# Optimization experiments

Hardware: AMD Instinct MI355X
Metric: run time of the kernel (lower is better)

The kernel has to match this reference:

```python
import jax, jax.numpy as jnp
import numpy as np

H_HEADS = 32
KV_HEADS = 8
HEAD_DIM = 128
HIDDEN = 2048
EPS = 1e-6


def rms_norm(x, w):
    # normalize over last dim (head_dim)
    var = jnp.mean(jnp.square(x), axis=-1, keepdims=True)
    return x * jax.lax.rsqrt(var + EPS) * w


def rotate_half(x):
    x1, x2 = jnp.split(x, 2, axis=-1)
    return jnp.concatenate([-x2, x1], axis=-1)


def setup_inputs() -> dict:
    key = jax.random.key(0)
    ks = jax.random.split(key, 8)
    B, Q, CTX = 1, 1024, 2048
    T = CTX + Q
    hidden_states = jax.random.normal(ks[0], (B, Q, HIDDEN), jnp.float32)
    target_hidden = jax.random.normal(ks[1], (B, CTX, HIDDEN), jnp.float32)
    # RoPE tables over the full concatenated length
    inv_freq = 1.0 / (10000.0 ** (np.arange(0, HEAD_DIM, 2, dtype=np.float32) / HEAD_DIM))
    pos = np.arange(T, dtype=np.float32)
    freqs = np.outer(pos, inv_freq)                     # [T, hd/2]
    emb = np.concatenate([freqs, freqs], axis=-1)       # [T, hd]
    cos = jnp.asarray(np.cos(emb))[None]                # [1, T, hd]
    sin = jnp.asarray(np.sin(emb))[None]
    # custom mask: context fully visible, causal within noise block
    noise_causal = jnp.tril(jnp.ones((Q, Q), bool))
    mask = jnp.concatenate([jnp.ones((Q, CTX), bool), noise_causal], axis=1)
    attention_mask = mask[None, None]                   # [1,1,Q,T]
    scale = 0.02
    wq = jax.random.normal(ks[2], (H_HEADS * HEAD_DIM, HIDDEN), jnp.float32) * scale
    wk = jax.random.normal(ks[3], (KV_HEADS * HEAD_DIM, HIDDEN), jnp.float32) * scale
    wv = jax.random.normal(ks[4], (KV_HEADS * HEAD_DIM, HIDDEN), jnp.float32) * scale
    wo = jax.random.normal(ks[5], (HIDDEN, H_HEADS * HEAD_DIM), jnp.float32) * scale
    q_norm_w = jnp.ones((HEAD_DIM,), jnp.float32)
    k_norm_w = jnp.ones((HEAD_DIM,), jnp.float32)
    return {"hidden_states": hidden_states, "target_hidden": target_hidden,
            "cos": cos, "sin": sin, "attention_mask": attention_mask,
            "wq": wq, "wk": wk, "wv": wv, "wo": wo,
            "q_norm_w": q_norm_w, "k_norm_w": k_norm_w}


def reference(hidden_states, target_hidden, cos, sin, attention_mask,
              wq, wk, wv, wo, q_norm_w, k_norm_w):
    B, Q, _ = hidden_states.shape
    CTX = target_hidden.shape[1]
    T = CTX + Q
    n_rep = H_HEADS // KV_HEADS
    scaling = HEAD_DIM ** -0.5

    # Q from noise tokens, QK-RMSNorm per head
    q = (hidden_states @ wq.T).reshape(B, Q, H_HEADS, HEAD_DIM)
    q = rms_norm(q, q_norm_w).transpose(0, 2, 1, 3)          # [B,H,Q,hd]

    # K/V: context then noise, concatenated along sequence
    k = jnp.concatenate([target_hidden @ wk.T, hidden_states @ wk.T], axis=1)
    k = rms_norm(k.reshape(B, T, KV_HEADS, HEAD_DIM), k_norm_w).transpose(0, 2, 1, 3)  # [B,Hk,T,hd]
    v = jnp.concatenate([target_hidden @ wv.T, hidden_states @ wv.T], axis=1)
    v = v.reshape(B, T, KV_HEADS, HEAD_DIM).transpose(0, 2, 1, 3)                       # [B,Hk,T,hd]

    # offset RoPE: K uses all T positions, Q uses the last Q positions
    cos_b = cos[:, None]                                      # [B,1,T,hd]
    sin_b = sin[:, None]
    q = q * cos_b[:, :, -Q:, :] + rotate_half(q) * sin_b[:, :, -Q:, :]
    k = k * cos_b + rotate_half(k) * sin_b

    # GQA attention without materializing repeated K/V
    qg = q.reshape(B, KV_HEADS, n_rep, Q, HEAD_DIM)
    scores = jnp.einsum('bgrqd,bgtd->bgrqt', qg, k) * scaling  # [B,Hk,rep,Q,T]
    scores = jnp.where(attention_mask[:, :, None], scores, jnp.finfo(scores.dtype).min)
    probs = jax.nn.softmax(scores, axis=-1)
    out = jnp.einsum('bgrqt,bgtd->bgrqd', probs, v)            # [B,Hk,rep,Q,hd]
    out = out.reshape(B, H_HEADS, Q, HEAD_DIM).transpose(0, 2, 1, 3).reshape(B, Q, H_HEADS * HEAD_DIM)
    return out @ wo.T
```

## Files before the change

### kernel.cpp

```cpp
#include <hip/hip_runtime.h>

#define HIDDEN 2048
#define NQ     1024
#define NCTX   2048
#define NTOT   3072
#define NHEADS 32
#define KVH    8
#define HD     128

typedef __attribute__((ext_vector_type(8))) __bf16 bf16x8;
typedef __attribute__((ext_vector_type(4))) __bf16 bf16x4;
typedef __attribute__((ext_vector_type(4))) float  f32x4;

#define MFMA16(a, b, c) __builtin_amdgcn_mfma_f32_16x16x32_bf16(a, b, c, 0, 0, 0)

#define MSTATIC 12.0f

__device__ __forceinline__ void load_lds16(const void* g, void* l) {
    __builtin_amdgcn_global_load_lds(
        (const __attribute__((address_space(1))) unsigned int*)g,
        (__attribute__((address_space(3))) unsigned int*)l, 16, 0, 0);
}

__global__ __launch_bounds__(256) void conv4_f32_bf16(const float* __restrict__ s0,
                                                      __bf16* __restrict__ d0, int n0,
                                                      const float* __restrict__ s1,
                                                      __bf16* __restrict__ d1, int n1,
                                                      const float* __restrict__ s2,
                                                      __bf16* __restrict__ d2, int n2,
                                                      const float* __restrict__ s3,
                                                      __bf16* __restrict__ d3, int n3) {
    const float* s; __bf16* d; int n;
    switch (blockIdx.y) {
        case 0:  s = s0; d = d0; n = n0; break;
        case 1:  s = s1; d = d1; n = n1; break;
        case 2:  s = s2; d = d2; n = n2; break;
        default: s = s3; d = d3; n = n3; break;
    }
    int i = blockIdx.x * 256 + threadIdx.x;
    int stride = gridDim.x * 256;
    for (; i < n; i += stride) {
        float4 v = ((const float4*)s)[i];
        bf16x4 o;
        o[0] = (__bf16)v.x; o[1] = (__bf16)v.y;
        o[2] = (__bf16)v.z; o[3] = (__bf16)v.w;
        ((bf16x4*)d)[i] = o;
    }
}

__global__ __launch_bounds__(256) void conv_wo(const float* __restrict__ wo,
                                               __bf16* __restrict__ w0,
                                               __bf16* __restrict__ w1) {
    int i = blockIdx.x * 256 + threadIdx.x;
    int stride = gridDim.x * 256;
    for (; i < 2048 * 1024; i += stride) {
        int r = i >> 10, cc = i & 1023;
        float4 v = ((const float4*)wo)[i];
        bf16x4 o;
        o[0] = (__bf16)v.x; o[1] = (__bf16)v.y;
        o[2] = (__bf16)v.z; o[3] = (__bf16)v.w;
        __bf16* dst = (cc & 512) ? w1 : w0;
        *(bf16x4*)(dst + (long)r * 2048 + (cc & 511) * 4) = o;
    }
}

__device__ __forceinline__ void gemm_compute64(const __bf16 (&As)[128][64],
                                               const __bf16 (&Bs)[128][64],
                                               f32x4 (&acc)[4][4],
                                               int wm, int wn, int n16, int quad, int rx) {
#pragma unroll
    for (int ks = 0; ks < 2; ks++) {
        bf16x8 af[4], bfr[4];
#pragma unroll
        for (int i = 0; i < 4; i++)
            af[i] = *(const bf16x8*)&As[wm + i * 16 + n16][((ks * 4 + quad) ^ rx) * 8];
#pragma unroll
        for (int j = 0; j < 4; j++)
            bfr[j] = *(const bf16x8*)&Bs[wn + j * 16 + n16][((ks * 4 + quad) ^ rx) * 8];
#pragma unroll
        for (int i = 0; i < 4; i++)
#pragma unroll
            for (int j = 0; j < 4; j++)
                acc[i][j] = MFMA16(af[i], bfr[j], acc[i][j]);
    }
}

template <typename OutT>
__device__ __forceinline__ void gemm_epilogue(const f32x4 (&acc)[4][4],
                                              OutT* __restrict__ Cblk, int ldc,
                                              int wm, int wn, int n16, int quad) {
#pragma unroll
    for (int i = 0; i < 4; i++)
#pragma unroll
        for (int j = 0; j < 4; j++)
#pragma unroll
            for (int r = 0; r < 4; r++)
                Cblk[(long)(wm + i * 16 + quad * 4 + r) * ldc + wn + j * 16 + n16] =
                    (OutT)acc[i][j][r];
}

template <typename OutT>
__device__ __forceinline__ void gemm128_bb(__bf16 (&As)[128][64], __bf16 (&Bs)[128][64],
                                           const __bf16* __restrict__ Ablk,
                                           const __bf16* __restrict__ Bblk,
                                           OutT* __restrict__ Cblk,
                                           int K, int lda, int ldb, int ldc) {
    const int tid  = threadIdx.x;
    const int lane = tid & 63;
    const int w    = tid >> 6;
    const int n16  = lane & 15;
    const int quad = lane >> 4;
    const int wm = (w & 1) * 64;
    const int wn = (w >> 1) * 64;

    f32x4 acc[4][4];
    const f32x4 fzero = {0.f, 0.f, 0.f, 0.f};
#pragma unroll
    for (int i = 0; i < 4; i++)
#pragma unroll
        for (int j = 0; j < 4; j++) acc[i][j] = fzero;

    const int srow  = w * 32 + (lane >> 3);
    const int sxor  = (lane >> 3) & 7;
    const int scol  = (lane & 7) * 8;
    const int sgcol = ((lane & 7) ^ sxor) * 8;
    const __bf16* Ap = Ablk + (long)srow * lda + sgcol;
    const __bf16* Bp = Bblk + (long)srow * ldb + sgcol;
    const int rx = n16 & 7;

    for (int k0 = 0; k0 < K; k0 += 64) {
#pragma unroll
        for (int i = 0; i < 4; i++) {
            load_lds16(Ap + (long)i * 8 * lda + k0, &As[srow + i * 8][scol]);
            load_lds16(Bp + (long)i * 8 * ldb + k0, &Bs[srow + i * 8][scol]);
        }
        __syncthreads();
        gemm_compute64(As, Bs, acc, wm, wn, n16, quad, rx);
        __syncthreads();
    }
    gemm_epilogue(acc, Cblk, ldc, wm, wn, n16, quad);
}

template <typename OutT>
__device__ __forceinline__ void gemm128_fb(__bf16 (&As)[128][64], __bf16 (&Bs)[128][64],
                                           const __bf16* __restrict__ Ablk,
                                           const float* __restrict__ Bblk,
                                           OutT* __restrict__ Cblk,
                                           int K, int lda, int ldb, int ldc) {
    const int tid  = threadIdx.x;
    const int lane = tid & 63;
    const int w    = tid >> 6;
    const int n16  = lane & 15;
    const int quad = lane >> 4;
    const int wm = (w & 1) * 64;
    const int wn = (w >> 1) * 64;

    f32x4 acc[4][4];
    const f32x4 fzero = {0.f, 0.f, 0.f, 0.f};
#pragma unroll
    for (int i = 0; i < 4; i++)
#pragma unroll
        for (int j = 0; j < 4; j++) acc[i][j] = fzero;

    const int srow  = w * 32 + (lane >> 3);
    const int sxor  = (lane >> 3) & 7;
    const int scol  = (lane & 7) * 8;
    const int sgcol = ((lane & 7) ^ sxor) * 8;
    const __bf16* Ap = Ablk + (long)srow * lda + sgcol;

    const int br0  = tid >> 3;
    const int bxor = br0 & 7;
    const int bgc  = (tid & 7) * 8;
    const int bwc  = ((tid & 7) ^ bxor) * 8;
    const float* Bptr = Bblk + (long)br0 * ldb + bgc;

    const int rx = n16 & 7;
    float4 breg[4][2];

#define LOAD_B(kk)                                                             \
    _Pragma("unroll") for (int i = 0; i < 4; i++) {                            \
        breg[i][0] = *(const float4*)(Bptr + (long)i * 32 * ldb + (kk));       \
        breg[i][1] = *(const float4*)(Bptr + (long)i * 32 * ldb + (kk) + 4);   \
    }

    LOAD_B(0);
    for (int k0 = 0; k0 < K; k0 += 64) {
#pragma unroll
        for (int i = 0; i < 4; i++)
            load_lds16(Ap + (long)i * 8 * lda + k0, &As[srow + i * 8][scol]);
#pragma unroll
        for (int i = 0; i < 4; i++) {
            bf16x8 bb;
            bb[0] = (__bf16)breg[i][0].x; bb[1] = (__bf16)breg[i][0].y;
            bb[2] = (__bf16)breg[i][0].z; bb[3] = (__bf16)breg[i][0].w;
            bb[4] = (__bf16)breg[i][1].x; bb[5] = (__bf16)breg[i][1].y;
            bb[6] = (__bf16)breg[i][1].z; bb[7] = (__bf16)breg[i][1].w;
            *(bf16x8*)&Bs[br0 + i * 32][bwc] = bb;
        }
        if (k0 + 64 < K) LOAD_B(k0 + 64);
        __syncthreads();
        gemm_compute64(As, Bs, acc, wm, wn, n16, quad, rx);
        __syncthreads();
    }
#undef LOAD_B
    gemm_epilogue(acc, Cblk, ldc, wm, wn, n16, quad);
}

__global__ __launch_bounds__(256) void gemm_kvq(const __bf16* __restrict__ tgtb,
                                                const __bf16* __restrict__ hidb,
                                                const __bf16* __restrict__ wkb,
                                                const __bf16* __restrict__ wvb,
                                                const float* __restrict__ wq,
                                                __bf16* __restrict__ kbf,
                                                __bf16* __restrict__ vbf,
                                                __bf16* __restrict__ qbf) {
    __shared__ __bf16 As[128][64];
    __shared__ __bf16 Bs[128][64];
    const int b = blockIdx.x;
    if (b < 384) {
        const int z = b / 192, bb = b - z * 192;
        const int n0 = (bb & 7) * 128, m0 = (bb >> 3) * 128;
        const __bf16* Ap = (m0 < 2048) ? tgtb + (long)m0 * 2048
                                       : hidb + (long)(m0 - 2048) * 2048;
        const __bf16* Bp = (z ? wvb : wkb) + (long)n0 * 2048;
        __bf16* Cp = (z ? vbf : kbf) + (long)m0 * 1024 + n0;
        gemm128_bb<__bf16>(As, Bs, Ap, Bp, Cp, 2048, 2048, 2048, 1024);
    } else {
        const int bb = b - 384;
        const int n0 = (bb & 31) * 128, m0 = (bb >> 5) * 128;
        gemm128_fb<__bf16>(As, Bs, hidb + (long)m0 * 2048, wq + (long)n0 * 2048,
                           qbf + (long)m0 * 4096 + n0, 2048, 2048, 2048, 4096);
    }
}

__global__ __launch_bounds__(256) void gemm_wo2(const __bf16* __restrict__ A,
                                                const __bf16* __restrict__ w0,
                                                const __bf16* __restrict__ w1,
                                                float* __restrict__ out,
                                                float* __restrict__ po1) {
    __shared__ __bf16 As[128][64];
    __shared__ __bf16 Bs[128][64];
    const int m0 = blockIdx.y * 128;
    const int n0 = blockIdx.x * 128;
    const int z  = blockIdx.z;
    const __bf16* Bp = (z ? w1 : w0) + (long)n0 * 2048;
    float* C = (z ? po1 : out) + (long)m0 * 2048 + n0;
    gemm128_bb<float>(As, Bs, A + (long)m0 * 4096 + z * 2048, Bp, C,
                      2048, 4096, 2048, 2048);
}

__global__ __launch_bounds__(256) void add2_inplace(float* __restrict__ out,
                                                    const float* __restrict__ p1, int n4) {
    int i = blockIdx.x * 256 + threadIdx.x;
    int stride = gridDim.x * 256;
    for (; i < n4; i += stride) {
        float4 a = ((const float4*)out)[i];
        float4 b = ((const float4*)p1)[i];
        float4 o;
        o.x = a.x + b.x; o.y = a.y + b.y;
        o.z = a.z + b.z; o.w = a.w + b.w;
        ((float4*)out)[i] = o;
    }
}

__global__ __launch_bounds__(256) void rmsnorm_rope2(__bf16* __restrict__ xq,
                                                     const float* __restrict__ wq,
                                                     __bf16* __restrict__ xk,
                                                     const float* __restrict__ wk,
                                                     const float* __restrict__ cosb,
                                                     const float* __restrict__ sinb) {
    const int z = blockIdx.y;
    __bf16*      x = z ? xk : xq;
    const float* w = z ? wk : wq;
    const int nheads     = z ? 8 : 32;
    const int row_stride = z ? 1024 : 4096;
    const int pos_offset = z ? 0 : 2048;
    const float outscale = z ? 1.0f : 0.08838834764831845f;
    const int nitems     = z ? 3072 * 8 : 1024 * 32;

    int item = blockIdx.x * 4 + (threadIdx.x >> 6);
    int lane = threadIdx.x & 63;
    if (item >= nitems) return;
    int row = item / nheads;
    int head = item - row * nheads;
    __bf16* p = x + (long)row * row_stride + head * HD;

    float x1 = (float)p[lane], x2 = (float)p[lane + 64];
    float ss = x1 * x1 + x2 * x2;
#pragma unroll
    for (int o = 32; o >= 1; o >>= 1) ss += __shfl_xor(ss, o);
    float r = rsqrtf(ss * (1.0f / 128.0f) + 1e-6f) * outscale;

    int pos = pos_offset + row;
    float c1 = cosb[pos * HD + lane], c2 = cosb[pos * HD + lane + 64];
    float s1 = sinb[pos * HD + lane], s2 = sinb[pos * HD + lane + 64];
    float y1 = x1 * r * w[lane];
    float y2 = x2 * r * w[lane + 64];
    p[lane]      = (__bf16)(y1 * c1 - y2 * s1);
    p[lane + 64] = (__bf16)(y2 * c2 + y1 * s2);
}

__global__ __launch_bounds__(256) void transpose_v(const __bf16* __restrict__ v,
                                                   __bf16* __restrict__ vt) {
    __shared__ __bf16 T[64][68];
    const int tid = threadIdx.x;
    const int t0 = blockIdx.x * 64;
    const int d0 = blockIdx.y * 64;
    const int g  = blockIdx.z;
    const __bf16* src = v + (long)t0 * 1024 + g * 128 + d0;
#pragma unroll
    for (int i = 0; i < 4; i++) {
        int idx = tid + i * 256;
        int r = idx >> 4, c4 = (idx & 15) * 4;
        *(bf16x4*)&T[r][c4] = *(const bf16x4*)(src + (long)r * 1024 + c4);
    }
    __syncthreads();
    __bf16* dst = vt + (long)g * 128 * 3072 + (long)d0 * 3072 + t0;
#pragma unroll
    for (int i = 0; i < 4; i++) {
        int idx = tid + i * 256;
        int r = idx >> 4, c4 = (idx & 15) * 4;
        bf16x4 o;
        o[0] = T[c4 + 0][r]; o[1] = T[c4 + 1][r];
        o[2] = T[c4 + 2][r]; o[3] = T[c4 + 3][r];
        *(bf16x4*)(dst + (long)r * 3072 + c4) = o;
    }
}

__global__ __launch_bounds__(256) void flash_attn_splitk(const __bf16* __restrict__ qb,
                                                         const __bf16* __restrict__ kb,
                                                         const __bf16* __restrict__ vtg,
                                                         __bf16* __restrict__ Opart0,
                                                         __bf16* __restrict__ Opart1,
                                                         float* __restrict__ lsum) {
    __shared__ __bf16 KsU[64 * 136];
    __shared__ __bf16 Vs[128][72];
#define KS(r, c) KsU[(r) * 136 + (c)]
#define PS(w_, m_, t_) KsU[(w_) * 2176 + (m_) * 68 + (t_)]

    const int tid  = threadIdx.x;
    const int lane = tid & 63;
    const int w    = tid >> 6;
    const int n    = lane & 15;
    const int quad = lane >> 4;

    const int bid = blockIdx.x;
    const int s   = blockIdx.y;
    const int g  = bid & 7;
    const int jj = bid >> 3;
    const int h  = g * 4 + (jj & 3);
    const int qt = jj >> 2;

    const int qr0 = qt * 128 + w * 16;

    bf16x8 qf[2][4];
#pragma unroll
    for (int mt = 0; mt < 2; mt++) {
        const __bf16* qp = qb + (long)(qr0 + mt * 64 + n) * 4096 + h * 128 + quad * 8;
        qf[mt][0] = *(const bf16x8*)(qp);
        qf[mt][1] = *(const bf16x8*)(qp + 32);
        qf[mt][2] = *(const bf16x8*)(qp + 64);
        qf[mt][3] = *(const bf16x8*)(qp + 96);
    }

    f32x4 O[2][8];
    const f32x4 fzero = {0.f, 0.f, 0.f, 0.f};
#pragma unroll
    for (int mt = 0; mt < 2; mt++)
#pragma unroll
        for (int dt = 0; dt < 8; dt++) O[mt][dt] = fzero;
    float l_loc[2] = {0.f, 0.f};

    const int ntot = 34 + 2 * qt;
    const int half = ntot >> 1;
    const int tbeg = s ? half : 0;
    const int tend = s ? ntot : half;

    const int krr = tid >> 4, kc8 = (tid & 15) * 8;
    const int vrr = tid >> 3, vc8 = (tid & 7) * 8;
    const __bf16* kp = kb + g * 128 + (long)(tbeg * 64 + krr) * 1024 + kc8;
    const __bf16* vp = vtg + (long)g * 128 * 3072 + (long)vrr * 3072 + tbeg * 64 + vc8;

    for (int tt = tbeg; tt < tend; tt++) {
#pragma unroll
        for (int i = 0; i < 4; i++)
            *(bf16x8*)&KS(krr + i * 16, kc8) = *(const bf16x8*)(kp + (long)i * 16 * 1024);
#pragma unroll
        for (int i = 0; i < 4; i++)
            *(bf16x8*)&Vs[vrr + i * 32][vc8] = *(const bf16x8*)(vp + (long)i * 32 * 3072);
        kp += 64 * 1024;
        vp += 64;
        __syncthreads();

        f32x4 S[2][4];
#pragma unroll
        for (int nt = 0; nt < 4; nt++) {
            f32x4 a0 = fzero, a1 = fzero;
#pragma unroll
            for (int ks = 0; ks < 4; ks++) {
                bf16x8 kf = *(const bf16x8*)&KS(nt * 16 + n, ks * 32 + quad * 8);
                a0 = MFMA16(kf, qf[0][ks], a0);
                a1 = MFMA16(kf, qf[1][ks], a1);
            }
            S[0][nt] = a0;
            S[1][nt] = a1;
        }

        if (tt >= ntot - 2) {
            const int t0 = tt * 64;
#pragma unroll
            for (int mt = 0; mt < 2; mt++) {
                const int lim = 2048 + qr0 + mt * 64 + n;
#pragma unroll
                for (int nt = 0; nt < 4; nt++)
#pragma unroll
                    for (int r = 0; r < 4; r++) {
                        int t = t0 + nt * 16 + quad * 4 + r;
                        if (t > lim) S[mt][nt][r] = -1e30f;
                    }
            }
        }

        __syncthreads();

#pragma unroll
        for (int mt = 0; mt < 2; mt++)
#pragma unroll
            for (int nt = 0; nt < 4; nt++)
#pragma unroll
                for (int r = 0; r < 4; r++) {
                    float p = __expf(S[mt][nt][r] - MSTATIC);
                    S[mt][nt][r] = p;
                    l_loc[mt] += p;
                }

#pragma unroll
        for (int mt = 0; mt < 2; mt++)
#pragma unroll
            for (int nt = 0; nt < 4; nt++) {
                bf16x4 pk;
#pragma unroll
                for (int r = 0; r < 4; r++) pk[r] = (__bf16)S[mt][nt][r];
                *(bf16x4*)&PS(w, mt * 16 + n, nt * 16 + quad * 4) = pk;
            }

        bf16x8 pa[2][2];
#pragma unroll
        for (int mt = 0; mt < 2; mt++)
#pragma unroll
            for (int kg = 0; kg < 2; kg++)
                pa[mt][kg] = *(const bf16x8*)&PS(w, mt * 16 + n, kg * 32 + quad * 8);

#pragma unroll
        for (int dt = 0; dt < 8; dt++) {
            bf16x8 vf0 = *(const bf16x8*)&Vs[dt * 16 + n][quad * 8];
            bf16x8 vf1 = *(const bf16x8*)&Vs[dt * 16 + n][32 + quad * 8];
#pragma unroll
            for (int mt = 0; mt < 2; mt++) {
                f32x4 acc = O[mt][dt];
                acc = MFMA16(pa[mt][0], vf0, acc);
                acc = MFMA16(pa[mt][1], vf1, acc);
                O[mt][dt] = acc;
            }
        }
        __syncthreads();
    }

#pragma unroll
    for (int mt = 0; mt < 2; mt++) {
        float sm = l_loc[mt];
        sm += __shfl_xor(sm, 16);
        sm += __shfl_xor(sm, 32);
        l_loc[mt] = sm;
    }

    __bf16* Op = s ? Opart1 : Opart0;
    const long tb = (long)(h * 8 + qt) * 128 * 128;
#pragma unroll
    for (int mt = 0; mt < 2; mt++)
#pragma unroll
        for (int dt = 0; dt < 8; dt++)
#pragma unroll
            for (int r = 0; r < 4; r++)
                Op[tb + (long)(mt * 64 + w * 16 + quad * 4 + r) * 128 + dt * 16 + n] =
                    (__bf16)O[mt][dt][r];
    if (quad == 0) {
        const int lb = (s * 256 + h * 8 + qt) * 128 + w * 16;
#pragma unroll
        for (int mt = 0; mt < 2; mt++)
            lsum[lb + mt * 64 + n] = l_loc[mt];
    }
#undef KS
#undef PS
}

__global__ __launch_bounds__(256) void flash_merge(const __bf16* __restrict__ O0,
                                                   const __bf16* __restrict__ O1,
                                                   const float* __restrict__ lsum,
                                                   __bf16* __restrict__ ob) {
    const int bx = blockIdx.x;
    const int h   = bx >> 4;
    const int r6  = bx & 15;
    const int qt  = r6 >> 1;
    const int sub = r6 & 1;
    const int row  = threadIdx.x >> 2;
    const int cseg = (threadIdx.x & 3) * 32;
    const int mrow = sub * 64 + row;

    const int tilei = h * 8 + qt;
    float inv = 1.0f / (lsum[tilei * 128 + mrow] + lsum[(256 + tilei) * 128 + mrow]);

    const long src = (long)tilei * 128 * 128 + (long)mrow * 128 + cseg;
    __bf16* dst = ob + (long)(qt * 128 + mrow) * 4096 + h * 128 + cseg;
#pragma unroll
    for (int j = 0; j < 4; j++) {
        bf16x8 x0 = *(const bf16x8*)(O0 + src + j * 8);
        bf16x8 x1 = *(const bf16x8*)(O1 + src + j * 8);
        bf16x8 o;
#pragma unroll
        for (int k = 0; k < 8; k++)
            o[k] = (__bf16)(((float)x0[k] + (float)x1[k]) * inv);
        *(bf16x8*)(dst + j * 8) = o;
    }
}

extern "C" void kernel_launch(void* const* d_in, const int* in_sizes, int n_in,
                              void* d_out, int out_size, void* d_ws, size_t ws_size,
                              hipStream_t stream) {
    const float* hidden = (const float*)d_in[0];
    const float* target = (const float*)d_in[1];
    const float* cosb   = (const float*)d_in[2];
    const float* sinb   = (const float*)d_in[3];
    const float* wq = (const float*)d_in[5];
    const float* wk = (const float*)d_in[6];
    const float* wv = (const float*)d_in[7];
    const float* wo = (const float*)d_in[8];
    const float* qw = (const float*)d_in[9];
    const float* kw = (const float*)d_in[10];
    float* out = (float*)d_out;

    char* ws = (char*)d_ws;
    const long MB = 1 << 20;
    __bf16* hidb = (__bf16*)(ws);
    __bf16* tgtb = (__bf16*)(ws + 4 * MB);
    __bf16* wkb  = (__bf16*)(ws + 12 * MB);
    __bf16* wvb  = (__bf16*)(ws + 16 * MB);
    __bf16* kbf  = (__bf16*)(ws + 20 * MB);
    __bf16* vbf  = (__bf16*)(ws + 26 * MB);
    __bf16* vtg  = (__bf16*)(ws + 32 * MB);
    float*  lbuf = (float*)(ws);
    __bf16* Op0  = (__bf16*)(ws + 4 * MB);
    __bf16* Op1  = (__bf16*)(ws + 12 * MB);
    __bf16* attnb= (__bf16*)(ws + 20 * MB);
    __bf16* wob0 = (__bf16*)(ws + 4 * MB);
    __bf16* wob1 = (__bf16*)(ws + 12 * MB);
    float*  po1  = (float*)(ws + 28 * MB);
    __bf16* qbf  = (__bf16*)d_out;

    dim3 blk(256);

    conv4_f32_bf16<<<dim3(1024, 4), blk, 0, stream>>>(
        hidden, hidb, (1024 * 2048) / 4, target, tgtb, (2048 * 2048) / 4,
        wk, wkb, (1024 * 2048) / 4, wv, wvb, (1024 * 2048) / 4);

    gemm_kvq<<<640, blk, 0, stream>>>(tgtb, hidb, wkb, wvb, wq, kbf, vbf, qbf);

    rmsnorm_rope2<<<dim3(8192, 2), blk, 0, stream>>>(qbf, qw, kbf, kw, cosb, sinb);

    transpose_v<<<dim3(48, 2, 8), blk, 0, stream>>>(vbf, vtg);

    flash_attn_splitk<<<dim3(256, 2), blk, 0, stream>>>(qbf, kbf, vtg, Op0, Op1, lbuf);
    flash_merge<<<512, blk, 0, stream>>>(Op0, Op1, lbuf, attnb);

    conv_wo<<<2048, blk, 0, stream>>>(wo, wob0, wob1);
    gemm_wo2<<<dim3(16, 8, 2), blk, 0, stream>>>(attnb, wob0, wob1, out, po1);
    add2_inplace<<<1024, blk, 0, stream>>>(out, po1, (1024 * 2048) / 4);
}
```

Before: 360.0 us.

## Shrink projection GEMM tiles to 128x64 and remap block IDs across XCDs

The K/V/Q projection GEMM and the output-projection GEMM now use 128x64 output tiles instead of 128x128. This doubles the block count (1280 and 512) so the work splits more evenly across the CUs. Linear block IDs are permuted with an XCD-aware stride mapping, and launch bounds request 5 blocks per CU. Each block now reads the A tile twice as often relative to the output it produces, which costs more global and LDS traffic per output element.

```diff
diff --git a/kernel.cpp b/kernel.cpp
--- a/kernel.cpp
+++ b/kernel.cpp
@@ -64,35 +64,35 @@
     }
 }
 
-__device__ __forceinline__ void gemm_compute64(const __bf16 (&As)[128][64],
-                                               const __bf16 (&Bs)[128][64],
-                                               f32x4 (&acc)[4][4],
-                                               int wm, int wn, int n16, int quad, int rx) {
+__device__ __forceinline__ void gemm_compute6432(const __bf16 (&As)[128][64],
+                                                 const __bf16 (&Bs)[64][64],
+                                                 f32x4 (&acc)[4][2],
+                                                 int wm, int wn, int n16, int quad, int rx) {
 #pragma unroll
     for (int ks = 0; ks < 2; ks++) {
-        bf16x8 af[4], bfr[4];
+        bf16x8 af[4], bfr[2];
 #pragma unroll
         for (int i = 0; i < 4; i++)
             af[i] = *(const bf16x8*)&As[wm + i * 16 + n16][((ks * 4 + quad) ^ rx) * 8];
 #pragma unroll
-        for (int j = 0; j < 4; j++)
+        for (int j = 0; j < 2; j++)
             bfr[j] = *(const bf16x8*)&Bs[wn + j * 16 + n16][((ks * 4 + quad) ^ rx) * 8];
 #pragma unroll
         for (int i = 0; i < 4; i++)
 #pragma unroll
-            for (int j = 0; j < 4; j++)
+            for (int j = 0; j < 2; j++)
                 acc[i][j] = MFMA16(af[i], bfr[j], acc[i][j]);
     }
 }
 
 template <typename OutT>
-__device__ __forceinline__ void gemm_epilogue(const f32x4 (&acc)[4][4],
+__device__ __forceinline__ void gemm_epilogue(const f32x4 (&acc)[4][2],
                                               OutT* __restrict__ Cblk, int ldc,
                                               int wm, int wn, int n16, int quad) {
 #pragma unroll
     for (int i = 0; i < 4; i++)
 #pragma unroll
-        for (int j = 0; j < 4; j++)
+        for (int j = 0; j < 2; j++)
 #pragma unroll
             for (int r = 0; r < 4; r++)
                 Cblk[(long)(wm + i * 16 + quad * 4 + r) * ldc + wn + j * 16 + n16] =
@@ -100,67 +100,69 @@
 }
 
 template <typename OutT>
-__device__ __forceinline__ void gemm128_bb(__bf16 (&As)[128][64], __bf16 (&Bs)[128][64],
-                                           const __bf16* __restrict__ Ablk,
-                                           const __bf16* __restrict__ Bblk,
-                                           OutT* __restrict__ Cblk,
-                                           int K, int lda, int ldb, int ldc) {
+__device__ __forceinline__ void gemm6432_bb(__bf16 (&As)[128][64], __bf16 (&Bs)[64][64],
+                                            const __bf16* __restrict__ Ablk,
+                                            const __bf16* __restrict__ Bblk,
+                                            OutT* __restrict__ Cblk,
+                                            int K, int lda, int ldb, int ldc) {
     const int tid  = threadIdx.x;
     const int lane = tid & 63;
     const int w    = tid >> 6;
     const int n16  = lane & 15;
     const int quad = lane >> 4;
     const int wm = (w & 1) * 64;
-    const int wn = (w >> 1) * 64;
-
-    f32x4 acc[4][4];
+    const int wn = (w >> 1) * 32;
+
+    f32x4 acc[4][2];
     const f32x4 fzero = {0.f, 0.f, 0.f, 0.f};
 #pragma unroll
     for (int i = 0; i < 4; i++)
 #pragma unroll
-        for (int j = 0; j < 4; j++) acc[i][j] = fzero;
+        for (int j = 0; j < 2; j++) acc[i][j] = fzero;
 
     const int srow  = w * 32 + (lane >> 3);
+    const int brow  = w * 16 + (lane >> 3);
     const int sxor  = (lane >> 3) & 7;
     const int scol  = (lane & 7) * 8;
     const int sgcol = ((lane & 7) ^ sxor) * 8;
     const __bf16* Ap = Ablk + (long)srow * lda + sgcol;
-    const __bf16* Bp = Bblk + (long)srow * ldb + sgcol;
+    const __bf16* Bp = Bblk + (long)brow * ldb + sgcol;
     const int rx = n16 & 7;
 
     for (int k0 = 0; k0 < K; k0 += 64) {
 #pragma unroll
-        for (int i = 0; i < 4; i++) {
+        for (int i = 0; i < 4; i++)
             load_lds16(Ap + (long)i * 8 * lda + k0, &As[srow + i * 8][scol]);
-            load_lds16(Bp + (long)i * 8 * ldb + k0, &Bs[srow + i * 8][scol]);
-        }
-        __syncthreads();
-        gemm_compute64(As, Bs, acc, wm, wn, n16, quad, rx);
+#pragma unroll
+        for (int i = 0; i < 2; i++)
+            load_lds16(Bp + (long)i * 8 * ldb + k0, &Bs[brow + i * 8][scol]);
+        __syncthreads();
+        gemm_compute6432(As, Bs, acc, wm, wn, n16, quad, rx);
         __syncthreads();
     }
     gemm_epilogue(acc, Cblk, ldc, wm, wn, n16, quad);
 }
 
 template <typename OutT>
-__device__ __forceinline__ void gemm128_fb(__bf16 (&As)[128][64], __bf16 (&Bs)[128][64],
-                                           const __bf16* __restrict__ Ablk,
-                                           const float* __restrict__ Bblk,
-                                           OutT* __restrict__ Cblk,
-                                           int K, int lda, int ldb, int ldc) {
+__device__ __forceinline__ void gemm6432_fb(__bf16 (&As)[128][64], __bf16 (&Bs)[64][64],
+                                            const __bf16* __restrict__ Ablk,
+                                            const float* __restrict__ Bblk,
+                                            OutT* __restrict__ Cblk,
+                                            int K, int lda, int ldb, int ldc) {
     const int tid  = threadIdx.x;
     const int lane = tid & 63;
     const int w    = tid >> 6;
     const int n16  = lane & 15;
     const int quad = lane >> 4;
     const int wm = (w & 1) * 64;
-    const int wn = (w >> 1) * 64;
-
-    f32x4 acc[4][4];
+    const int wn = (w >> 1) * 32;
+
+    f32x4 acc[4][2];
     const f32x4 fzero = {0.f, 0.f, 0.f, 0.f};
 #pragma unroll
     for (int i = 0; i < 4; i++)
 #pragma unroll
-        for (int j = 0; j < 4; j++) acc[i][j] = fzero;
+        for (int j = 0; j < 2; j++) acc[i][j] = fzero;
 
     const int srow  = w * 32 + (lane >> 3);
     const int sxor  = (lane >> 3) & 7;
@@ -175,10 +177,10 @@
     const float* Bptr = Bblk + (long)br0 * ldb + bgc;
 
     const int rx = n16 & 7;
-    float4 breg[4][2];
+    float4 breg[2][2];
 
 #define LOAD_B(kk)                                                             \
-    _Pragma("unroll") for (int i = 0; i < 4; i++) {                            \
+    _Pragma("unroll") for (int i = 0; i < 2; i++) {                            \
         breg[i][0] = *(const float4*)(Bptr + (long)i * 32 * ldb + (kk));       \
         breg[i][1] = *(const float4*)(Bptr + (long)i * 32 * ldb + (kk) + 4);   \
     }
@@ -189,7 +191,7 @@
         for (int i = 0; i < 4; i++)
             load_lds16(Ap + (long)i * 8 * lda + k0, &As[srow + i * 8][scol]);
 #pragma unroll
-        for (int i = 0; i < 4; i++) {
+        for (int i = 0; i < 2; i++) {
             bf16x8 bb;
             bb[0] = (__bf16)breg[i][0].x; bb[1] = (__bf16)breg[i][0].y;
             bb[2] = (__bf16)breg[i][0].z; bb[3] = (__bf16)breg[i][0].w;
@@ -199,54 +201,56 @@
         }
         if (k0 + 64 < K) LOAD_B(k0 + 64);
         __syncthreads();
-        gemm_compute64(As, Bs, acc, wm, wn, n16, quad, rx);
+        gemm_compute6432(As, Bs, acc, wm, wn, n16, quad, rx);
         __syncthreads();
     }
 #undef LOAD_B
     gemm_epilogue(acc, Cblk, ldc, wm, wn, n16, quad);
 }
 
-__global__ __launch_bounds__(256) void gemm_kvq(const __bf16* __restrict__ tgtb,
-                                                const __bf16* __restrict__ hidb,
-                                                const __bf16* __restrict__ wkb,
-                                                const __bf16* __restrict__ wvb,
-                                                const float* __restrict__ wq,
-                                                __bf16* __restrict__ kbf,
-                                                __bf16* __restrict__ vbf,
-                                                __bf16* __restrict__ qbf) {
+__global__ __launch_bounds__(256, 5) void gemm_kvq(const __bf16* __restrict__ tgtb,
+                                                   const __bf16* __restrict__ hidb,
+                                                   const __bf16* __restrict__ wkb,
+                                                   const __bf16* __restrict__ wvb,
+                                                   const float* __restrict__ wq,
+                                                   __bf16* __restrict__ kbf,
+                                                   __bf16* __restrict__ vbf,
+                                                   __bf16* __restrict__ qbf) {
     __shared__ __bf16 As[128][64];
-    __shared__ __bf16 Bs[128][64];
-    const int b = blockIdx.x;
-    if (b < 384) {
-        const int z = b / 192, bb = b - z * 192;
-        const int n0 = (bb & 7) * 128, m0 = (bb >> 3) * 128;
+    __shared__ __bf16 Bs[64][64];
+    const int bid = blockIdx.x;
+    const int b = (bid & 7) * 160 + (bid >> 3);
+    if (b < 768) {
+        const int z = b >> 9 ? 1 : (b >= 384), t = b - z * 384;
+        const int m0 = (t >> 4) * 128, n0 = (t & 15) * 64;
         const __bf16* Ap = (m0 < 2048) ? tgtb + (long)m0 * 2048
                                        : hidb + (long)(m0 - 2048) * 2048;
         const __bf16* Bp = (z ? wvb : wkb) + (long)n0 * 2048;
         __bf16* Cp = (z ? vbf : kbf) + (long)m0 * 1024 + n0;
-        gemm128_bb<__bf16>(As, Bs, Ap, Bp, Cp, 2048, 2048, 2048, 1024);
+        gemm6432_bb<__bf16>(As, Bs, Ap, Bp, Cp, 2048, 2048, 2048, 1024);
     } else {
-        const int bb = b - 384;
-        const int n0 = (bb & 31) * 128, m0 = (bb >> 5) * 128;
-        gemm128_fb<__bf16>(As, Bs, hidb + (long)m0 * 2048, wq + (long)n0 * 2048,
-                           qbf + (long)m0 * 4096 + n0, 2048, 2048, 2048, 4096);
-    }
-}
-
-__global__ __launch_bounds__(256) void gemm_wo2(const __bf16* __restrict__ A,
-                                                const __bf16* __restrict__ w0,
-                                                const __bf16* __restrict__ w1,
-                                                float* __restrict__ out,
-                                                float* __restrict__ po1) {
+        const int t = b - 768;
+        const int m0 = (t >> 6) * 128, n0 = (t & 63) * 64;
+        gemm6432_fb<__bf16>(As, Bs, hidb + (long)m0 * 2048, wq + (long)n0 * 2048,
+                            qbf + (long)m0 * 4096 + n0, 2048, 2048, 2048, 4096);
+    }
+}
+
+__global__ __launch_bounds__(256, 5) void gemm_wo2(const __bf16* __restrict__ A,
+                                                   const __bf16* __restrict__ w0,
+                                                   const __bf16* __restrict__ w1,
+                                                   float* __restrict__ out,
+                                                   float* __restrict__ po1) {
     __shared__ __bf16 As[128][64];
-    __shared__ __bf16 Bs[128][64];
-    const int m0 = blockIdx.y * 128;
-    const int n0 = blockIdx.x * 128;
-    const int z  = blockIdx.z;
+    __shared__ __bf16 Bs[64][64];
+    const int bid = blockIdx.x;
+    const int b = (bid & 7) * 64 + (bid >> 3);
+    const int z = b >> 8, t = b & 255;
+    const int m0 = (t >> 5) * 128, n0 = (t & 31) * 64;
     const __bf16* Bp = (z ? w1 : w0) + (long)n0 * 2048;
     float* C = (z ? po1 : out) + (long)m0 * 2048 + n0;
-    gemm128_bb<float>(As, Bs, A + (long)m0 * 4096 + z * 2048, Bp, C,
-                      2048, 4096, 2048, 2048);
+    gemm6432_bb<float>(As, Bs, A + (long)m0 * 4096 + z * 2048, Bp, C,
+                       2048, 4096, 2048, 2048);
 }
 
 __global__ __launch_bounds__(256) void add2_inplace(float* __restrict__ out,
@@ -563,7 +567,7 @@
         hidden, hidb, (1024 * 2048) / 4, target, tgtb, (2048 * 2048) / 4,
         wk, wkb, (1024 * 2048) / 4, wv, wvb, (1024 * 2048) / 4);
 
-    gemm_kvq<<<640, blk, 0, stream>>>(tgtb, hidb, wkb, wvb, wq, kbf, vbf, qbf);
+    gemm_kvq<<<1280, blk, 0, stream>>>(tgtb, hidb, wkb, wvb, wq, kbf, vbf, qbf);
 
     rmsnorm_rope2<<<dim3(8192, 2), blk, 0, stream>>>(qbf, qw, kbf, kw, cosb, sinb);
 
@@ -573,6 +577,6 @@
     flash_merge<<<512, blk, 0, stream>>>(Op0, Op1, lbuf, attnb);
 
     conv_wo<<<2048, blk, 0, stream>>>(wo, wob0, wob1);
-    gemm_wo2<<<dim3(16, 8, 2), blk, 0, stream>>>(attnb, wob0, wob1, out, po1);
+    gemm_wo2<<<512, blk, 0, stream>>>(attnb, wob0, wob1, out, po1);
     add2_inplace<<<1024, blk, 0, stream>>>(out, po1, (1024 * 2048) / 4);
 }
```

Measured after the change: 358.4 us. No clear change (-0.4%).

## Retile GEMMs to 256x64 blocks, fuse wo conversion, split-K four ways

Applied to the files above, without the earlier changes.

Replaces the 128x128 GEMM tiles with 256x64 tiles, each wave owning 64 rows and sharing a 64-wide B tile, and remaps block indices so neighbouring blocks share A or B panels. The separate wo fp32-to-bf16 conversion kernel is removed. The output projection now reads fp32 wo directly and converts it in registers while staging it into shared memory. The output GEMM is split four ways along K into 512 blocks with four partial buffers summed by a four-way add kernel. This cuts one kernel launch and the round-trip write of converted weights, and raises block count for occupancy, at the cost of extra partial-sum traffic and more A reloads per output tile.

```diff
diff --git a/kernel.cpp b/kernel.cpp
--- a/kernel.cpp
+++ b/kernel.cpp
@@ -48,26 +48,10 @@
     }
 }
 
-__global__ __launch_bounds__(256) void conv_wo(const float* __restrict__ wo,
-                                               __bf16* __restrict__ w0,
-                                               __bf16* __restrict__ w1) {
-    int i = blockIdx.x * 256 + threadIdx.x;
-    int stride = gridDim.x * 256;
-    for (; i < 2048 * 1024; i += stride) {
-        int r = i >> 10, cc = i & 1023;
-        float4 v = ((const float4*)wo)[i];
-        bf16x4 o;
-        o[0] = (__bf16)v.x; o[1] = (__bf16)v.y;
-        o[2] = (__bf16)v.z; o[3] = (__bf16)v.w;
-        __bf16* dst = (cc & 512) ? w1 : w0;
-        *(bf16x4*)(dst + (long)r * 2048 + (cc & 511) * 4) = o;
-    }
-}
-
-__device__ __forceinline__ void gemm_compute64(const __bf16 (&As)[128][64],
-                                               const __bf16 (&Bs)[128][64],
-                                               f32x4 (&acc)[4][4],
-                                               int wm, int wn, int n16, int quad, int rx) {
+__device__ __forceinline__ void gemm_compute256(const __bf16 (&As)[256][64],
+                                                const __bf16 (&Bs)[64][64],
+                                                f32x4 (&acc)[4][4],
+                                                int wm, int n16, int quad, int rx) {
 #pragma unroll
     for (int ks = 0; ks < 2; ks++) {
         bf16x8 af[4], bfr[4];
@@ -76,7 +60,7 @@
             af[i] = *(const bf16x8*)&As[wm + i * 16 + n16][((ks * 4 + quad) ^ rx) * 8];
 #pragma unroll
         for (int j = 0; j < 4; j++)
-            bfr[j] = *(const bf16x8*)&Bs[wn + j * 16 + n16][((ks * 4 + quad) ^ rx) * 8];
+            bfr[j] = *(const bf16x8*)&Bs[j * 16 + n16][((ks * 4 + quad) ^ rx) * 8];
 #pragma unroll
         for (int i = 0; i < 4; i++)
 #pragma unroll
@@ -86,32 +70,31 @@
 }
 
 template <typename OutT>
-__device__ __forceinline__ void gemm_epilogue(const f32x4 (&acc)[4][4],
-                                              OutT* __restrict__ Cblk, int ldc,
-                                              int wm, int wn, int n16, int quad) {
+__device__ __forceinline__ void gemm_epi256(const f32x4 (&acc)[4][4],
+                                            OutT* __restrict__ Cblk, int ldc,
+                                            int wm, int n16, int quad) {
 #pragma unroll
     for (int i = 0; i < 4; i++)
 #pragma unroll
         for (int j = 0; j < 4; j++)
 #pragma unroll
             for (int r = 0; r < 4; r++)
-                Cblk[(long)(wm + i * 16 + quad * 4 + r) * ldc + wn + j * 16 + n16] =
+                Cblk[(long)(wm + i * 16 + quad * 4 + r) * ldc + j * 16 + n16] =
                     (OutT)acc[i][j][r];
 }
 
 template <typename OutT>
-__device__ __forceinline__ void gemm128_bb(__bf16 (&As)[128][64], __bf16 (&Bs)[128][64],
-                                           const __bf16* __restrict__ Ablk,
-                                           const __bf16* __restrict__ Bblk,
-                                           OutT* __restrict__ Cblk,
-                                           int K, int lda, int ldb, int ldc) {
+__device__ __forceinline__ void gemm25664_bb(__bf16 (&As)[256][64], __bf16 (&Bs)[64][64],
+                                             const __bf16* __restrict__ Ablk,
+                                             const __bf16* __restrict__ Bblk,
+                                             OutT* __restrict__ Cblk,
+                                             int K, int lda, int ldb, int ldc) {
     const int tid  = threadIdx.x;
     const int lane = tid & 63;
     const int w    = tid >> 6;
     const int n16  = lane & 15;
     const int quad = lane >> 4;
-    const int wm = (w & 1) * 64;
-    const int wn = (w >> 1) * 64;
+    const int wm   = w * 64;
 
     f32x4 acc[4][4];
     const f32x4 fzero = {0.f, 0.f, 0.f, 0.f};
@@ -120,40 +103,41 @@
 #pragma unroll
         for (int j = 0; j < 4; j++) acc[i][j] = fzero;
 
-    const int srow  = w * 32 + (lane >> 3);
+    const int arow  = w * 64 + (lane >> 3);
+    const int brow  = w * 16 + (lane >> 3);
     const int sxor  = (lane >> 3) & 7;
     const int scol  = (lane & 7) * 8;
     const int sgcol = ((lane & 7) ^ sxor) * 8;
-    const __bf16* Ap = Ablk + (long)srow * lda + sgcol;
-    const __bf16* Bp = Bblk + (long)srow * ldb + sgcol;
+    const __bf16* Ap = Ablk + (long)arow * lda + sgcol;
+    const __bf16* Bp = Bblk + (long)brow * ldb + sgcol;
     const int rx = n16 & 7;
 
     for (int k0 = 0; k0 < K; k0 += 64) {
 #pragma unroll
-        for (int i = 0; i < 4; i++) {
-            load_lds16(Ap + (long)i * 8 * lda + k0, &As[srow + i * 8][scol]);
-            load_lds16(Bp + (long)i * 8 * ldb + k0, &Bs[srow + i * 8][scol]);
-        }
-        __syncthreads();
-        gemm_compute64(As, Bs, acc, wm, wn, n16, quad, rx);
-        __syncthreads();
-    }
-    gemm_epilogue(acc, Cblk, ldc, wm, wn, n16, quad);
+        for (int i = 0; i < 8; i++)
+            load_lds16(Ap + (long)i * 8 * lda + k0, &As[arow + i * 8][scol]);
+#pragma unroll
+        for (int i = 0; i < 2; i++)
+            load_lds16(Bp + (long)i * 8 * ldb + k0, &Bs[brow + i * 8][scol]);
+        __syncthreads();
+        gemm_compute256(As, Bs, acc, wm, n16, quad, rx);
+        __syncthreads();
+    }
+    gemm_epi256(acc, Cblk, ldc, wm, n16, quad);
 }
 
 template <typename OutT>
-__device__ __forceinline__ void gemm128_fb(__bf16 (&As)[128][64], __bf16 (&Bs)[128][64],
-                                           const __bf16* __restrict__ Ablk,
-                                           const float* __restrict__ Bblk,
-                                           OutT* __restrict__ Cblk,
-                                           int K, int lda, int ldb, int ldc) {
+__device__ __forceinline__ void gemm25664_fb(__bf16 (&As)[256][64], __bf16 (&Bs)[64][64],
+                                             const __bf16* __restrict__ Ablk,
+                                             const float* __restrict__ Bblk,
+                                             OutT* __restrict__ Cblk,
+                                             int K, int lda, int ldb, int ldc) {
     const int tid  = threadIdx.x;
     const int lane = tid & 63;
     const int w    = tid >> 6;
     const int n16  = lane & 15;
     const int quad = lane >> 4;
-    const int wm = (w & 1) * 64;
-    const int wn = (w >> 1) * 64;
+    const int wm   = w * 64;
 
     f32x4 acc[4][4];
     const f32x4 fzero = {0.f, 0.f, 0.f, 0.f};
@@ -162,103 +146,117 @@
 #pragma unroll
         for (int j = 0; j < 4; j++) acc[i][j] = fzero;
 
-    const int srow  = w * 32 + (lane >> 3);
+    const int arow  = w * 64 + (lane >> 3);
     const int sxor  = (lane >> 3) & 7;
     const int scol  = (lane & 7) * 8;
     const int sgcol = ((lane & 7) ^ sxor) * 8;
-    const __bf16* Ap = Ablk + (long)srow * lda + sgcol;
-
-    const int br0  = tid >> 3;
-    const int bxor = br0 & 7;
-    const int bgc  = (tid & 7) * 8;
-    const int bwc  = ((tid & 7) ^ bxor) * 8;
-    const float* Bptr = Bblk + (long)br0 * ldb + bgc;
+    const __bf16* Ap = Ablk + (long)arow * lda + sgcol;
+
+    const int brr  = tid >> 2;
+    const int bc0  = (tid & 3) * 16;
+    const int bch  = (tid & 3) * 2;
+    const int bxor = brr & 7;
+    const float* Bptr = Bblk + (long)brr * ldb + bc0;
 
     const int rx = n16 & 7;
-    float4 breg[4][2];
+    float4 breg[4];
 
 #define LOAD_B(kk)                                                             \
-    _Pragma("unroll") for (int i = 0; i < 4; i++) {                            \
-        breg[i][0] = *(const float4*)(Bptr + (long)i * 32 * ldb + (kk));       \
-        breg[i][1] = *(const float4*)(Bptr + (long)i * 32 * ldb + (kk) + 4);   \
-    }
+    _Pragma("unroll") for (int i = 0; i < 4; i++)                              \
+        breg[i] = *(const float4*)(Bptr + (kk) + i * 4);
 
     LOAD_B(0);
     for (int k0 = 0; k0 < K; k0 += 64) {
 #pragma unroll
-        for (int i = 0; i < 4; i++)
-            load_lds16(Ap + (long)i * 8 * lda + k0, &As[srow + i * 8][scol]);
-#pragma unroll
-        for (int i = 0; i < 4; i++) {
-            bf16x8 bb;
-            bb[0] = (__bf16)breg[i][0].x; bb[1] = (__bf16)breg[i][0].y;
-            bb[2] = (__bf16)breg[i][0].z; bb[3] = (__bf16)breg[i][0].w;
-            bb[4] = (__bf16)breg[i][1].x; bb[5] = (__bf16)breg[i][1].y;
-            bb[6] = (__bf16)breg[i][1].z; bb[7] = (__bf16)breg[i][1].w;
-            *(bf16x8*)&Bs[br0 + i * 32][bwc] = bb;
+        for (int i = 0; i < 8; i++)
+            load_lds16(Ap + (long)i * 8 * lda + k0, &As[arow + i * 8][scol]);
+        {
+            bf16x8 b0, b1;
+#pragma unroll
+            for (int j = 0; j < 4; j++) {
+                b0[j]     = (__bf16)breg[0][j]; b0[j + 4] = (__bf16)breg[1][j];
+                b1[j]     = (__bf16)breg[2][j]; b1[j + 4] = (__bf16)breg[3][j];
+            }
+            *(bf16x8*)&Bs[brr][((bch + 0) ^ bxor) * 8] = b0;
+            *(bf16x8*)&Bs[brr][((bch + 1) ^ bxor) * 8] = b1;
         }
         if (k0 + 64 < K) LOAD_B(k0 + 64);
         __syncthreads();
-        gemm_compute64(As, Bs, acc, wm, wn, n16, quad, rx);
+        gemm_compute256(As, Bs, acc, wm, n16, quad, rx);
         __syncthreads();
     }
 #undef LOAD_B
-    gemm_epilogue(acc, Cblk, ldc, wm, wn, n16, quad);
-}
-
-__global__ __launch_bounds__(256) void gemm_kvq(const __bf16* __restrict__ tgtb,
-                                                const __bf16* __restrict__ hidb,
-                                                const __bf16* __restrict__ wkb,
-                                                const __bf16* __restrict__ wvb,
-                                                const float* __restrict__ wq,
-                                                __bf16* __restrict__ kbf,
-                                                __bf16* __restrict__ vbf,
-                                                __bf16* __restrict__ qbf) {
-    __shared__ __bf16 As[128][64];
-    __shared__ __bf16 Bs[128][64];
-    const int b = blockIdx.x;
+    gemm_epi256(acc, Cblk, ldc, wm, n16, quad);
+}
+
+__global__ __launch_bounds__(256, 4) void gemm_kvq(const __bf16* __restrict__ tgtb,
+                                                   const __bf16* __restrict__ hidb,
+                                                   const __bf16* __restrict__ wkb,
+                                                   const __bf16* __restrict__ wvb,
+                                                   const float* __restrict__ wq,
+                                                   __bf16* __restrict__ kbf,
+                                                   __bf16* __restrict__ vbf,
+                                                   __bf16* __restrict__ qbf) {
+    __shared__ __bf16 As[256][64];
+    __shared__ __bf16 Bs[64][64];
+    const int bid = blockIdx.x;
+    const int b = (bid & 7) * 80 + (bid >> 3);
     if (b < 384) {
-        const int z = b / 192, bb = b - z * 192;
-        const int n0 = (bb & 7) * 128, m0 = (bb >> 3) * 128;
+        const int z = b >= 192, t = b - z * 192;
+        const int m0 = (t >> 4) * 256, n0 = (t & 15) * 64;
         const __bf16* Ap = (m0 < 2048) ? tgtb + (long)m0 * 2048
                                        : hidb + (long)(m0 - 2048) * 2048;
         const __bf16* Bp = (z ? wvb : wkb) + (long)n0 * 2048;
         __bf16* Cp = (z ? vbf : kbf) + (long)m0 * 1024 + n0;
-        gemm128_bb<__bf16>(As, Bs, Ap, Bp, Cp, 2048, 2048, 2048, 1024);
+        gemm25664_bb<__bf16>(As, Bs, Ap, Bp, Cp, 2048, 2048, 2048, 1024);
     } else {
-        const int bb = b - 384;
-        const int n0 = (bb & 31) * 128, m0 = (bb >> 5) * 128;
-        gemm128_fb<__bf16>(As, Bs, hidb + (long)m0 * 2048, wq + (long)n0 * 2048,
-                           qbf + (long)m0 * 4096 + n0, 2048, 2048, 2048, 4096);
-    }
-}
-
-__global__ __launch_bounds__(256) void gemm_wo2(const __bf16* __restrict__ A,
-                                                const __bf16* __restrict__ w0,
-                                                const __bf16* __restrict__ w1,
-                                                float* __restrict__ out,
-                                                float* __restrict__ po1) {
-    __shared__ __bf16 As[128][64];
-    __shared__ __bf16 Bs[128][64];
-    const int m0 = blockIdx.y * 128;
-    const int n0 = blockIdx.x * 128;
-    const int z  = blockIdx.z;
-    const __bf16* Bp = (z ? w1 : w0) + (long)n0 * 2048;
-    float* C = (z ? po1 : out) + (long)m0 * 2048 + n0;
-    gemm128_bb<float>(As, Bs, A + (long)m0 * 4096 + z * 2048, Bp, C,
-                      2048, 4096, 2048, 2048);
-}
-
-__global__ __launch_bounds__(256) void add2_inplace(float* __restrict__ out,
-                                                    const float* __restrict__ p1, int n4) {
+        const int t = b - 384;
+        const int m0 = (t >> 6) * 256, n0 = (t & 63) * 64;
+        gemm25664_fb<__bf16>(As, Bs, hidb + (long)m0 * 2048, wq + (long)n0 * 2048,
+                             qbf + (long)m0 * 4096 + n0, 2048, 2048, 2048, 4096);
+    }
+}
+
+__global__ __launch_bounds__(256, 4) void gemm_wo4(const __bf16* __restrict__ A,
+                                                   const float* __restrict__ wo,
+                                                   float* __restrict__ out,
+                                                   float* __restrict__ p1,
+                                                   float* __restrict__ p2,
+                                                   float* __restrict__ p3) {
+    __shared__ __bf16 As[256][64];
+    __shared__ __bf16 Bs[64][64];
+    const int bid = blockIdx.x;
+    const int b = (bid & 7) * 64 + (bid >> 3);
+    const int z = b >> 7, t = b & 127;
+    const int m0 = (t >> 5) * 256, n0 = (t & 31) * 64;
+    float* C;
+    switch (z) {
+        case 0:  C = out; break;
+        case 1:  C = p1;  break;
+        case 2:  C = p2;  break;
+        default: C = p3;  break;
+    }
+    gemm25664_fb<float>(As, Bs, A + (long)m0 * 4096 + z * 1024,
+                        wo + (long)n0 * 4096 + z * 1024,
+                        C + (long)m0 * 2048 + n0, 1024, 4096, 4096, 2048);
+}
+
+__global__ __launch_bounds__(256) void add4_wo(float* __restrict__ out,
+                                               const float* __restrict__ p1,
+                                               const float* __restrict__ p2,
+                                               const float* __restrict__ p3, int n4) {
     int i = blockIdx.x * 256 + threadIdx.x;
     int stride = gridDim.x * 256;
     for (; i < n4; i += stride) {
         float4 a = ((const float4*)out)[i];
         float4 b = ((const float4*)p1)[i];
+        float4 c = ((const float4*)p2)[i];
+        float4 d = ((const float4*)p3)[i];
         float4 o;
-        o.x = a.x + b.x; o.y = a.y + b.y;
-        o.z = a.z + b.z; o.w = a.w + b.w;
+        o.x = (a.x + b.x) + (c.x + d.x);
+        o.y = (a.y + b.y) + (c.y + d.y);
+        o.z = (a.z + b.z) + (c.z + d.z);
+        o.w = (a.w + b.w) + (c.w + d.w);
         ((float4*)out)[i] = o;
     }
 }
@@ -552,9 +550,9 @@
     __bf16* Op0  = (__bf16*)(ws + 4 * MB);
     __bf16* Op1  = (__bf16*)(ws + 12 * MB);
     __bf16* attnb= (__bf16*)(ws + 20 * MB);
-    __bf16* wob0 = (__bf16*)(ws + 4 * MB);
-    __bf16* wob1 = (__bf16*)(ws + 12 * MB);
-    float*  po1  = (float*)(ws + 28 * MB);
+    float*  po1  = (float*)(ws + 4 * MB);
+    float*  po2  = (float*)(ws + 12 * MB);
+    float*  po3  = (float*)(ws + 28 * MB);
     __bf16* qbf  = (__bf16*)d_out;
 
     dim3 blk(256);
@@ -572,7 +570,6 @@
     flash_attn_splitk<<<dim3(256, 2), blk, 0, stream>>>(qbf, kbf, vtg, Op0, Op1, lbuf);
     flash_merge<<<512, blk, 0, stream>>>(Op0, Op1, lbuf, attnb);
 
-    conv_wo<<<2048, blk, 0, stream>>>(wo, wob0, wob1);
-    gemm_wo2<<<dim3(16, 8, 2), blk, 0, stream>>>(attnb, wob0, wob1, out, po1);
-    add2_inplace<<<1024, blk, 0, stream>>>(out, po1, (1024 * 2048) / 4);
-}
+    gemm_wo4<<<512, blk, 0, stream>>>(attnb, wo, out, po1, po2, po3);
+    add4_wo<<<1024, blk, 0, stream>>>(out, po1, po2, po3, (1024 * 2048) / 4);
+}
```

After: 338.6 us. 5.9% less time.
